# Performance work log

Measured on AMD Instinct MI355X. Metric: run time of the kernel, lower is better.

Reference implementation:

```python
import jax, jax.numpy as jnp
from jax import lax
import numpy as np

LBDA = 0.1


def otam_cum_dist(dists, lbda=LBDA):
    """OTAM cumulative distance, dists: [Q, S, L, M] -> [Q, S].

    Matches the torch reference: pad last dim by 1 on each side with zeros,
    then run the banded soft-min (temperature lbda) DP recurrence. We use
    logaddexp for the stable form of -lbda*log(sum(exp(-x/lbda))).
    """
    Q, S, L, M = dists.shape
    d = jnp.pad(dists, ((0, 0), (0, 0), (0, 0), (1, 1)))  # [Q,S,L,M+2]

    # Row 0: cum[0,0]=0, cum[0,m]=sum_{k=1..m} d[0,k]  (prefix sum)
    zero_col = jnp.zeros((Q, S, 1), d.dtype)
    row0 = jnp.concatenate([zero_col, jnp.cumsum(d[:, :, 0, 1:], axis=-1)], axis=-1)

    # For m = 1 .. M+1: boundary columns (m==1 and m==M+1) add the
    # extra exp(-cum[l-1, m]/lbda) term.
    is_bnd = np.zeros(M + 1, dtype=bool)
    is_bnd[0] = True
    is_bnd[-1] = True
    is_bnd = jnp.asarray(is_bnd)

    def row_step(prev_row, d_row):
        # prev_row, d_row: [Q, S, M+2]
        def col_step(prev_cur, xs):
            d_lm, pr_m1, pr_m, bnd = xs  # each [Q,S] (bnd scalar)
            s = jnp.logaddexp(-pr_m1 / lbda, -prev_cur / lbda)
            s = jnp.where(bnd, jnp.logaddexp(s, -pr_m / lbda), s)
            cur = d_lm - lbda * s
            return cur, cur

        xs = (
            jnp.moveaxis(d_row[:, :, 1:], -1, 0),        # d[l, m],     m=1..M+1
            jnp.moveaxis(prev_row[:, :, :-1], -1, 0),    # cum[l-1,m-1]
            jnp.moveaxis(prev_row[:, :, 1:], -1, 0),     # cum[l-1,m]
            is_bnd,
        )
        zero = jnp.zeros(d_row.shape[:2], d_row.dtype)
        _, cols = lax.scan(col_step, zero, xs)           # [M+1, Q, S]
        new_row = jnp.concatenate([zero[..., None], jnp.moveaxis(cols, 0, -1)], axis=-1)
        return new_row, None

    d_rows = jnp.moveaxis(d[:, :, 1:, :], 2, 0)          # [L-1, Q, S, M+2]
    last_row, _ = lax.scan(row_step, row0, d_rows)
    return last_row[:, :, -1]


def setup_inputs() -> dict:
    key = jax.random.key(0)
    similarity = jax.random.uniform(key, (400, 400, 16, 16), dtype=jnp.float32)
    return {"similarity": similarity}


def reference(similarity):
    distance = 1.0 - similarity
    votes = otam_cum_dist(distance) + otam_cum_dist(
        jnp.transpose(distance, (0, 1, 3, 2))
    )
    votes = votes * 0.5
    return -votes
```

## Files before the change

### kernel.cpp

```cpp
#include <hip/hip_runtime.h>


#define KSC 14.426950408889634f
#define CL2 0.06931471805599453f

#if __has_builtin(__builtin_amdgcn_exp2f)
static __device__ __forceinline__ float fexp2(float x) { return __builtin_amdgcn_exp2f(x); }
#else
static __device__ __forceinline__ float fexp2(float x) {
    float r; asm("v_exp_f32 %0, %1" : "=v"(r) : "v"(x)); return r;
}
#endif
#if __has_builtin(__builtin_amdgcn_logf)
static __device__ __forceinline__ float flog2(float x) { return __builtin_amdgcn_logf(x); }
#else
static __device__ __forceinline__ float flog2(float x) {
    float r; asm("v_log_f32 %0, %1" : "=v"(r) : "v"(x)); return r;
}
#endif

static __device__ __forceinline__ float sm2(float a, float b) {
    float mn = fminf(a, b), mx = fmaxf(a, b);
    float e  = fexp2((mn - mx) * KSC);
    return mn - CL2 * flog2(1.0f + e);
}

static __device__ __forceinline__ float sm3(float a, float b, float c) {
    float mn = fminf(fminf(a, b), c);
    float s  = fexp2((mn - a) * KSC)
             + fexp2((mn - b) * KSC)
             + fexp2((mn - c) * KSC);
    return mn - CL2 * flog2(s);
}

#define UNPACK(r, b0, b1, b2, b3)                                          \
    r[0]=1.0f-b0.x;  r[1]=1.0f-b0.y;  r[2]=1.0f-b0.z;  r[3]=1.0f-b0.w;     \
    r[4]=1.0f-b1.x;  r[5]=1.0f-b1.y;  r[6]=1.0f-b1.z;  r[7]=1.0f-b1.w;     \
    r[8]=1.0f-b2.x;  r[9]=1.0f-b2.y;  r[10]=1.0f-b2.z; r[11]=1.0f-b2.w;    \
    r[12]=1.0f-b3.x; r[13]=1.0f-b3.y; r[14]=1.0f-b3.z; r[15]=1.0f-b3.w

__global__ __launch_bounds__(64) void otam_kernel(const float* __restrict__ sim,
                                                  float* __restrict__ out,
                                                  int npairs) {
    int p = blockIdx.x * 64 + threadIdx.x;
    if (p >= npairs) return;
    const float4* tp = (const float4*)(sim + (size_t)p * 256);

    float prev[18], S[16], r[16];

    float4 a0 = tp[0],  a1 = tp[1],  a2 = tp[2],  a3 = tp[3];
    float4 b0 = tp[4],  b1 = tp[5],  b2 = tp[6],  b3 = tp[7];
    float4 c0 = tp[8],  c1 = tp[9],  c2 = tp[10], c3 = tp[11];

    UNPACK(r, a0, a1, a2, a3);

    prev[0] = 0.0f;
#pragma unroll
    for (int m = 1; m <= 16; ++m) prev[m] = prev[m - 1] + r[m - 1];
    prev[17] = prev[16];

    {
        float cur = r[0];
        S[0] = cur;
#pragma unroll
        for (int i = 1; i < 16; ++i) {
            cur  = r[i] + sm3(0.0f, 0.0f, cur);
            S[i] = cur;
        }
    }

    for (int l = 1; l < 16; ++l) {
        a0 = b0; a1 = b1; a2 = b2; a3 = b3;
        b0 = c0; b1 = c1; b2 = c2; b3 = c3;
        if (l + 2 < 16) {
            c0 = tp[(l + 2) * 4 + 0];
            c1 = tp[(l + 2) * 4 + 1];
            c2 = tp[(l + 2) * 4 + 2];
            c3 = tp[(l + 2) * 4 + 3];
        }
        UNPACK(r, a0, a1, a2, a3);

        {
            float a_old = prev[0];
            float t     = prev[1];
            float fcur  = r[0] + sm3(a_old, 0.0f, t);
            prev[1]     = fcur;
            a_old       = t;
#pragma unroll
            for (int m = 2; m <= 16; ++m) {
                t       = prev[m];
                fcur    = r[m - 1] + sm2(a_old, fcur);
                prev[m] = fcur;
                a_old   = t;
            }
            prev[17] = sm3(a_old, fcur, prev[17]);
        }

        {
            float po   = S[0];
            float scur = S[0] + r[0];
            S[0] = scur;
#pragma unroll
            for (int i = 1; i < 16; ++i) {
                float t2 = S[i];
                scur = r[i] + sm2(po, t2);
                S[i] = scur;
                po   = t2;
            }
        }
    }

    {
        float po  = S[0];
        float cur = S[0];
#pragma unroll
        for (int i = 1; i < 16; ++i) {
            float t = S[i];
            cur = sm3(po, t, cur);
            po  = t;
        }
        out[p] = -0.5f * (prev[17] + cur);
    }
}

extern "C" void kernel_launch(void* const* d_in, const int* in_sizes, int n_in,
                              void* d_out, int out_size, void* d_ws, size_t ws_size,
                              hipStream_t stream) {
    const float* sim = (const float*)d_in[0];
    float* out       = (float*)d_out;
    int npairs = in_sizes[0] / 256;
    int blocks = (npairs + 63) / 64;
    otam_kernel<<<blocks, 64, 0, stream>>>(sim, out, npairs);
}
```

Before: 233.4 us.

## Split the two OTAM directions across two wavefronts and rescale to log2 domain

```diff
diff --git a/kernel.cpp b/kernel.cpp
--- a/kernel.cpp
+++ b/kernel.cpp
@@ -1,8 +1,8 @@
 #include <hip/hip_runtime.h>
 
 
-#define KSC 14.426950408889634f
-#define CL2 0.06931471805599453f
+#define KSC  14.426950408889634f
+#define HCL2 0.034657359027997264f
 
 #if __has_builtin(__builtin_amdgcn_exp2f)
 static __device__ __forceinline__ float fexp2(float x) { return __builtin_amdgcn_exp2f(x); }
@@ -19,107 +19,115 @@
 }
 #endif
 
-static __device__ __forceinline__ float sm2(float a, float b) {
-    float mn = fminf(a, b), mx = fmaxf(a, b);
-    float e  = fexp2((mn - mx) * KSC);
-    return mn - CL2 * flog2(1.0f + e);
+static __device__ __forceinline__ float lse2(float x, float y) {
+    float mx = fmaxf(x, y), mn = fminf(x, y);
+    return mx + flog2(1.0f + fexp2(mn - mx));
+}
+static __device__ __forceinline__ float lse3(float x, float y, float z) {
+    float mx = fmaxf(fmaxf(x, y), z);
+    float s  = fexp2(x - mx) + fexp2(y - mx) + fexp2(z - mx);
+    return mx + flog2(s);
 }
 
-static __device__ __forceinline__ float sm3(float a, float b, float c) {
-    float mn = fminf(fminf(a, b), c);
-    float s  = fexp2((mn - a) * KSC)
-             + fexp2((mn - b) * KSC)
-             + fexp2((mn - c) * KSC);
-    return mn - CL2 * flog2(s);
-}
+#define UNPACKK(rk, b0, b1, b2, b3)                                              \
+    rk[0]=(b0.x-1.0f)*KSC;  rk[1]=(b0.y-1.0f)*KSC;  rk[2]=(b0.z-1.0f)*KSC;       \
+    rk[3]=(b0.w-1.0f)*KSC;  rk[4]=(b1.x-1.0f)*KSC;  rk[5]=(b1.y-1.0f)*KSC;       \
+    rk[6]=(b1.z-1.0f)*KSC;  rk[7]=(b1.w-1.0f)*KSC;  rk[8]=(b2.x-1.0f)*KSC;       \
+    rk[9]=(b2.y-1.0f)*KSC;  rk[10]=(b2.z-1.0f)*KSC; rk[11]=(b2.w-1.0f)*KSC;      \
+    rk[12]=(b3.x-1.0f)*KSC; rk[13]=(b3.y-1.0f)*KSC; rk[14]=(b3.z-1.0f)*KSC;      \
+    rk[15]=(b3.w-1.0f)*KSC
 
-#define UNPACK(r, b0, b1, b2, b3)                                          \
-    r[0]=1.0f-b0.x;  r[1]=1.0f-b0.y;  r[2]=1.0f-b0.z;  r[3]=1.0f-b0.w;     \
-    r[4]=1.0f-b1.x;  r[5]=1.0f-b1.y;  r[6]=1.0f-b1.z;  r[7]=1.0f-b1.w;     \
-    r[8]=1.0f-b2.x;  r[9]=1.0f-b2.y;  r[10]=1.0f-b2.z; r[11]=1.0f-b2.w;    \
-    r[12]=1.0f-b3.x; r[13]=1.0f-b3.y; r[14]=1.0f-b3.z; r[15]=1.0f-b3.w
+#define PIPE_ADVANCE(l)                                                          \
+    b0 = c0; b1 = c1; b2 = c2; b3 = c3;                                          \
+    c0 = e0; c1 = e1; c2 = e2; c3 = e3;                                          \
+    if ((l) + 2 < 16) {                                                          \
+        e0 = tp[((l) + 2) * 4 + 0]; e1 = tp[((l) + 2) * 4 + 1];                  \
+        e2 = tp[((l) + 2) * 4 + 2]; e3 = tp[((l) + 2) * 4 + 3];                  \
+    }
 
-__global__ __launch_bounds__(64) void otam_kernel(const float* __restrict__ sim,
-                                                  float* __restrict__ out,
-                                                  int npairs) {
-    int p = blockIdx.x * 64 + threadIdx.x;
-    if (p >= npairs) return;
+__global__ __launch_bounds__(128) void otam_kernel(const float* __restrict__ sim,
+                                                   float* __restrict__ out,
+                                                   int npairs) {
+    __shared__ float tshare[64];
+    const int lane = threadIdx.x & 63;
+    const int wid  = threadIdx.x >> 6;
+    int p = blockIdx.x * 64 + lane;
+    if (p >= npairs) p = npairs - 1;
     const float4* tp = (const float4*)(sim + (size_t)p * 256);
 
-    float prev[18], S[16], r[16];
+    float rk[16];
+    float4 b0 = tp[0], b1 = tp[1], b2 = tp[2],  b3 = tp[3];
+    float4 c0 = tp[4], c1 = tp[5], c2 = tp[6],  c3 = tp[7];
+    float4 e0 = tp[8], e1 = tp[9], e2 = tp[10], e3 = tp[11];
 
-    float4 a0 = tp[0],  a1 = tp[1],  a2 = tp[2],  a3 = tp[3];
-    float4 b0 = tp[4],  b1 = tp[5],  b2 = tp[6],  b3 = tp[7];
-    float4 c0 = tp[8],  c1 = tp[9],  c2 = tp[10], c3 = tp[11];
+    UNPACKK(rk, b0, b1, b2, b3);
 
-    UNPACK(r, a0, a1, a2, a3);
+    float resu;
+    if (wid == 0) {
+        float up[18];
+        up[0] = 0.0f;
+#pragma unroll
+        for (int m = 1; m <= 16; ++m) up[m] = up[m - 1] + rk[m - 1];
+        up[17] = up[16];
 
-    prev[0] = 0.0f;
+        for (int l = 1; l < 16; ++l) {
+            PIPE_ADVANCE(l);
+            UNPACKK(rk, b0, b1, b2, b3);
+            float t   = up[1];
+            float cur = lse3(0.0f, 0.0f, t) + rk[0];
+            up[1] = cur;
+            float a_old = t;
 #pragma unroll
-    for (int m = 1; m <= 16; ++m) prev[m] = prev[m - 1] + r[m - 1];
-    prev[17] = prev[16];
-
-    {
-        float cur = r[0];
-        S[0] = cur;
+            for (int m = 2; m <= 16; ++m) {
+                t      = up[m];
+                cur    = lse2(a_old, cur) + rk[m - 1];
+                up[m]  = cur;
+                a_old  = t;
+            }
+            up[17] = lse3(a_old, cur, up[17]);
+        }
+        resu = up[17];
+    } else {
+        float S[16];
+        {
+            float cur = rk[0];
+            S[0] = cur;
 #pragma unroll
-        for (int i = 1; i < 16; ++i) {
-            cur  = r[i] + sm3(0.0f, 0.0f, cur);
-            S[i] = cur;
+            for (int i = 1; i < 16; ++i) {
+                cur  = lse3(0.0f, 0.0f, cur) + rk[i];
+                S[i] = cur;
+            }
         }
+        for (int l = 1; l < 16; ++l) {
+            PIPE_ADVANCE(l);
+            UNPACKK(rk, b0, b1, b2, b3);
+            float po  = S[0];
+            float cur = S[0] + rk[0];
+            S[0] = cur;
+#pragma unroll
+            for (int i = 1; i < 16; ++i) {
+                float t = S[i];
+                cur  = lse2(po, t) + rk[i];
+                S[i] = cur;
+                po   = t;
+            }
+        }
+        {
+            float po = S[0], cur = S[0];
+#pragma unroll
+            for (int i = 1; i < 16; ++i) {
+                float t = S[i];
+                cur = lse3(po, t, cur);
+                po  = t;
+            }
+            tshare[lane] = cur;
+        }
+        resu = 0.0f;
     }
 
-    for (int l = 1; l < 16; ++l) {
-        a0 = b0; a1 = b1; a2 = b2; a3 = b3;
-        b0 = c0; b1 = c1; b2 = c2; b3 = c3;
-        if (l + 2 < 16) {
-            c0 = tp[(l + 2) * 4 + 0];
-            c1 = tp[(l + 2) * 4 + 1];
-            c2 = tp[(l + 2) * 4 + 2];
-            c3 = tp[(l + 2) * 4 + 3];
-        }
-        UNPACK(r, a0, a1, a2, a3);
-
-        {
-            float a_old = prev[0];
-            float t     = prev[1];
-            float fcur  = r[0] + sm3(a_old, 0.0f, t);
-            prev[1]     = fcur;
-            a_old       = t;
-#pragma unroll
-            for (int m = 2; m <= 16; ++m) {
-                t       = prev[m];
-                fcur    = r[m - 1] + sm2(a_old, fcur);
-                prev[m] = fcur;
-                a_old   = t;
-            }
-            prev[17] = sm3(a_old, fcur, prev[17]);
-        }
-
-        {
-            float po   = S[0];
-            float scur = S[0] + r[0];
-            S[0] = scur;
-#pragma unroll
-            for (int i = 1; i < 16; ++i) {
-                float t2 = S[i];
-                scur = r[i] + sm2(po, t2);
-                S[i] = scur;
-                po   = t2;
-            }
-        }
-    }
-
-    {
-        float po  = S[0];
-        float cur = S[0];
-#pragma unroll
-        for (int i = 1; i < 16; ++i) {
-            float t = S[i];
-            cur = sm3(po, t, cur);
-            po  = t;
-        }
-        out[p] = -0.5f * (prev[17] + cur);
+    __syncthreads();
+    if (wid == 0) {
+        out[p] = HCL2 * (resu + tshare[lane]);
     }
 }
 
@@ -130,5 +138,5 @@
     float* out       = (float*)d_out;
     int npairs = in_sizes[0] / 256;
     int blocks = (npairs + 63) / 64;
-    otam_kernel<<<blocks, 64, 0, stream>>>(sim, out, npairs);
+    otam_kernel<<<blocks, 128, 0, stream>>>(sim, out, npairs);
 }
```

Result: no change. 236.4 us (+1.3%).
